# Optimization experiments

Hardware: AMD Instinct MI355X
Metric: run time of the kernel (lower is better)

The kernel has to match this reference:

```python
import jax, jax.numpy as jnp
import numpy as np

B, S, E, H = 2, 2048, 1024, 16
D = E // H  # head dimension = 64


def setup_inputs() -> dict:
    key = jax.random.key(0)
    ks = jax.random.split(key, 12)
    scale_in = 1.0 / np.sqrt(E)
    x = jax.random.normal(ks[0], (B, S, E), dtype=jnp.float32)
    # random 0/1 attention mask (1 = attend, 0 = masked out)
    mask = jax.random.randint(ks[1], (B, S, S), 0, 2, dtype=jnp.int32)
    # per-head QKV projections, stacked over the head axis: [H, E, D]
    Wq = jax.random.normal(ks[2], (H, E, D), dtype=jnp.float32) * scale_in
    bq = jnp.zeros((H, D), dtype=jnp.float32)
    Wk = jax.random.normal(ks[3], (H, E, D), dtype=jnp.float32) * scale_in
    bk = jnp.zeros((H, D), dtype=jnp.float32)
    Wv = jax.random.normal(ks[4], (H, E, D), dtype=jnp.float32) * scale_in
    bv = jnp.zeros((H, D), dtype=jnp.float32)
    # output projection: [H*D, E] == [E, E]
    Wo = jax.random.normal(ks[5], (H * D, E), dtype=jnp.float32) * scale_in
    bo = jnp.zeros((E,), dtype=jnp.float32)
    return {"x": x, "mask": mask, "Wq": Wq, "bq": bq, "Wk": Wk, "bk": bk,
            "Wv": Wv, "bv": bv, "Wo": Wo, "bo": bo}


def reference(x, mask, Wq, bq, Wk, bk, Wv, bv, Wo, bo):
    # Batched equivalent of the per-head Python loop: all heads at once.
    q = jnp.einsum('bse,hed->bhsd', x, Wq) + bq[None, :, None, :]  # [B,H,S,D]
    k = jnp.einsum('bse,hed->bhsd', x, Wk) + bk[None, :, None, :]
    v = jnp.einsum('bse,hed->bhsd', x, Wv) + bv[None, :, None, :]
    scale = 1.0 / jnp.sqrt(jnp.asarray(D, dtype=q.dtype))
    scores = jnp.einsum('bhsd,bhtd->bhst', q, k) * scale          # [B,H,S,S]
    scores = jnp.where(mask[:, None, :, :] != 0, scores, jnp.asarray(-1e9, scores.dtype))
    attn = jax.nn.softmax(scores, axis=-1)
    ctx = jnp.einsum('bhst,bhtd->bhsd', attn, v)                  # [B,H,S,D]
    # concat heads along feature dim (torch.cat(dim=2))
    concat = jnp.transpose(ctx, (0, 2, 1, 3)).reshape(B, S, H * D)
    return concat @ Wo + bo
```

## Files before the change

kernel.cpp:

```cpp
#include <hip/hip_runtime.h>

#define S_LEN 2048
#define EMB   1024
#define NH    16
#define HD    64
#define BS    2
#define QSCALE 0.18033688f

typedef __bf16 bf16;
typedef bf16  bf16x8 __attribute__((ext_vector_type(8)));
typedef bf16  bf16x4 __attribute__((ext_vector_type(4)));
typedef float f32x4  __attribute__((ext_vector_type(4)));
typedef unsigned long long u64;
typedef unsigned int u32;

__device__ __forceinline__ bf16x8 ld8(const bf16* p){ return *(const bf16x8*)p; }

__device__ __forceinline__ void gl_lds16(const bf16* g, void* l) {
    __builtin_amdgcn_global_load_lds(
        (const __attribute__((address_space(1))) void*)g,
        (__attribute__((address_space(3))) void*)l,
        16, 0, 0);
}

#define SW(row, g) ((((g) ^ ((row) & 7))) * 8)

__global__ __launch_bounds__(256)
void pack_mask(const int* __restrict__ mask, u64* __restrict__ pm)
{
    int lane = threadIdx.x & 63;
    int row  = blockIdx.x * 4 + (threadIdx.x >> 6);
    const int* mr = mask + (size_t)row * S_LEN;
    u64* pr = pm + (size_t)row * (S_LEN / 64);
    for (int i = 0; i < S_LEN / 64; ++i) {
        u64 bits = __ballot(mr[i * 64 + lane] != 0);
        if (lane == 0) pr[i] = bits;
    }
}

__global__ __launch_bounds__(256)
void transpose_w(const float* __restrict__ W0, const float* __restrict__ W1,
                 const float* __restrict__ W2, const float* __restrict__ W3,
                 bf16* __restrict__ Wt)
{
    const int z = blockIdx.z;
    const float* W = z == 0 ? W0 : z == 1 ? W1 : z == 2 ? W2 : W3;
    const bool head = z < 3;
    const int k0 = blockIdx.x * 64, n0 = blockIdx.y * 64;
    const int tid = threadIdx.x;
    __shared__ float T[64][68];
    {
        int k = k0 + (tid >> 2), cg = (tid & 3) * 16;
        size_t base = head ? ((size_t)(n0 >> 6) * ((size_t)EMB * HD) + (size_t)k * HD + cg)
                           : ((size_t)k * EMB + n0 + cg);
        #pragma unroll
        for (int g = 0; g < 4; ++g) {
            f32x4 v = *(const f32x4*)(W + base + g * 4);
            #pragma unroll
            for (int j = 0; j < 4; ++j) T[tid >> 2][cg + g * 4 + j] = v[j];
        }
    }
    __syncthreads();
    {
        int n = n0 + (tid >> 2), ck = (tid & 3) * 16;
        bf16 t16[16];
        #pragma unroll
        for (int j = 0; j < 16; ++j) t16[j] = (bf16)T[ck + j][tid >> 2];
        bf16* outp = Wt + (size_t)z * EMB * EMB + (size_t)n * EMB + k0 + ck;
        *(bf16x8*)outp       = *(bf16x8*)t16;
        *(bf16x8*)(outp + 8) = *(bf16x8*)(t16 + 8);
    }
}

__global__ __launch_bounds__(256)
void cvt_f32_bf16(const float* __restrict__ x, bf16* __restrict__ y)
{
    size_t i = ((size_t)blockIdx.x * 256 + threadIdx.x) * 16;
    bf16 t[16];
    #pragma unroll
    for (int g = 0; g < 4; ++g) {
        f32x4 v = *(const f32x4*)(x + i + g * 4);
        #pragma unroll
        for (int j = 0; j < 4; ++j) t[g * 4 + j] = (bf16)v[j];
    }
    *(bf16x8*)(y + i)     = *(bf16x8*)t;
    *(bf16x8*)(y + i + 8) = *(bf16x8*)(t + 8);
}

__global__ __launch_bounds__(256)
void scale_q(bf16* __restrict__ q)
{
    size_t i = ((size_t)blockIdx.x * 256 + threadIdx.x) * 8;
    bf16x8 v = *(bf16x8*)(q + i);
    #pragma unroll
    for (int j = 0; j < 8; ++j) v[j] = (bf16)((float)v[j] * QSCALE);
    *(bf16x8*)(q + i) = v;
}

__global__ __launch_bounds__(256, 3)
void gemm_qkv(const void* __restrict__ Ap, const bf16* __restrict__ Wt,
              const float* __restrict__ bqp, const float* __restrict__ bkp,
              const float* __restrict__ bvp,
              bf16* __restrict__ qb, bf16* __restrict__ kb, bf16* __restrict__ VT,
              int a32)
{
    const int tid  = threadIdx.x;
    const int lane = tid & 63, quad = lane >> 4, c = lane & 15;
    const int w = tid >> 6, wm = w >> 1, wn = w & 1;
    const int m0 = blockIdx.x * 128;
    const int n0 = blockIdx.y * 128;

    __shared__ bf16 Ash[128][64];
    __shared__ bf16 Wsh[128][64];

    f32x4 acc[4][4];
    #pragma unroll
    for (int mt = 0; mt < 4; ++mt)
        #pragma unroll
        for (int nt = 0; nt < 4; ++nt) acc[mt][nt] = (f32x4){0.f,0.f,0.f,0.f};

    const int lrow = lane >> 3, lcol = (lane & 7) * 8;

    for (int k0 = 0; k0 < EMB; k0 += 64) {
        __syncthreads();
        if (!a32) {
            const bf16* A = (const bf16*)Ap;
            #pragma unroll
            for (int j = 0; j < 4; ++j)
                gl_lds16(A + (size_t)(m0 + w * 32 + j * 8 + lrow) * EMB + k0 + lcol,
                         &Ash[w * 32 + j * 8][0]);
        } else {
            const float* A = (const float*)Ap + (size_t)(m0 + (tid >> 1)) * EMB + k0 + (tid & 1) * 32;
            bf16 t[32];
            #pragma unroll
            for (int g = 0; g < 8; ++g) {
                f32x4 v = *(const f32x4*)(A + g * 4);
                #pragma unroll
                for (int j = 0; j < 4; ++j) t[g * 4 + j] = (bf16)v[j];
            }
            #pragma unroll
            for (int g2 = 0; g2 < 4; ++g2)
                *(bf16x8*)&Ash[tid >> 1][(tid & 1) * 32 + g2 * 8] = *(bf16x8*)(t + g2 * 8);
        }
        #pragma unroll
        for (int j = 0; j < 4; ++j)
            gl_lds16(Wt + (size_t)(n0 + w * 32 + j * 8 + lrow) * EMB + k0 + lcol,
                     &Wsh[w * 32 + j * 8][0]);
        __syncthreads();

        #pragma unroll
        for (int kh = 0; kh < 2; ++kh) {
            bf16x8 af[4], bfv[4];
            #pragma unroll
            for (int mt = 0; mt < 4; ++mt) af[mt]  = ld8(&Ash[wm * 64 + mt * 16 + c][kh * 32 + quad * 8]);
            #pragma unroll
            for (int nt = 0; nt < 4; ++nt) bfv[nt] = ld8(&Wsh[wn * 64 + nt * 16 + c][kh * 32 + quad * 8]);
            #pragma unroll
            for (int mt = 0; mt < 4; ++mt)
                #pragma unroll
                for (int nt = 0; nt < 4; ++nt)
                    acc[mt][nt] = __builtin_amdgcn_mfma_f32_16x16x32_bf16(af[mt], bfv[nt], acc[mt][nt], 0, 0, 0);
        }
    }

    const int z = n0 >> 10;
    const float* bias = z == 0 ? bqp : z == 1 ? bkp : bvp;
    #pragma unroll
    for (int nt = 0; nt < 4; ++nt) {
        int nn = (n0 & 1023) + wn * 64 + nt * 16 + c;
        float bv_ = bias[nn];
        #pragma unroll
        for (int mt = 0; mt < 4; ++mt)
            #pragma unroll
            for (int r = 0; r < 4; ++r) {
                int m = m0 + wm * 64 + mt * 16 + quad * 4 + r;
                float v = acc[mt][nt][r] + bv_;
                if (z == 0)      qb[(size_t)m * EMB + nn] = (bf16)(v * QSCALE);
                else if (z == 1) kb[(size_t)m * EMB + nn] = (bf16)v;
                else {
                    int head = nn >> 6, d = nn & 63;
                    VT[((size_t)((m >> 11) * NH + head) * HD + d) * S_LEN + (m & 2047)] = (bf16)v;
                }
            }
    }
}

__global__ __launch_bounds__(256, 4)
void gemm_o(const bf16* __restrict__ Ap, const bf16* __restrict__ Wt,
            const float* __restrict__ bo, float* __restrict__ C)
{
    const int tid  = threadIdx.x;
    const int lane = tid & 63, quad = lane >> 4, c = lane & 15;
    const int w = tid >> 6, wm = w >> 1, wn = w & 1;
    const int m0 = blockIdx.x * 128;
    const int n0 = blockIdx.y * 64;

    __shared__ bf16 Ash[128][64];
    __shared__ bf16 Wsh[64][64];

    f32x4 acc[4][2];
    #pragma unroll
    for (int mt = 0; mt < 4; ++mt)
        #pragma unroll
        for (int nt = 0; nt < 2; ++nt) acc[mt][nt] = (f32x4){0.f,0.f,0.f,0.f};

    const int lrow = lane >> 3, lcol = (lane & 7) * 8;

    for (int k0 = 0; k0 < EMB; k0 += 64) {
        __syncthreads();
        #pragma unroll
        for (int j = 0; j < 4; ++j)
            gl_lds16(Ap + (size_t)(m0 + w * 32 + j * 8 + lrow) * EMB + k0 + lcol,
                     &Ash[w * 32 + j * 8][0]);
        #pragma unroll
        for (int j = 0; j < 2; ++j)
            gl_lds16(Wt + (size_t)(n0 + w * 16 + j * 8 + lrow) * EMB + k0 + lcol,
                     &Wsh[w * 16 + j * 8][0]);
        __syncthreads();

        #pragma unroll
        for (int kh = 0; kh < 2; ++kh) {
            bf16x8 af[4], bfv[2];
            #pragma unroll
            for (int mt = 0; mt < 4; ++mt) af[mt]  = ld8(&Ash[wm * 64 + mt * 16 + c][kh * 32 + quad * 8]);
            #pragma unroll
            for (int nt = 0; nt < 2; ++nt) bfv[nt] = ld8(&Wsh[wn * 32 + nt * 16 + c][kh * 32 + quad * 8]);
            #pragma unroll
            for (int mt = 0; mt < 4; ++mt)
                #pragma unroll
                for (int nt = 0; nt < 2; ++nt)
                    acc[mt][nt] = __builtin_amdgcn_mfma_f32_16x16x32_bf16(af[mt], bfv[nt], acc[mt][nt], 0, 0, 0);
        }
    }

    #pragma unroll
    for (int nt = 0; nt < 2; ++nt) {
        int n = n0 + wn * 32 + nt * 16 + c;
        float bv_ = bo[n];
        #pragma unroll
        for (int mt = 0; mt < 4; ++mt)
            #pragma unroll
            for (int r = 0; r < 4; ++r) {
                int m = m0 + wm * 64 + mt * 16 + quad * 4 + r;
                C[(size_t)m * EMB + n] = acc[mt][nt][r] + bv_;
            }
    }
}

__global__ __launch_bounds__(512)
void gemm128(const void* __restrict__ Ap, const float* __restrict__ Wp,
             const bf16* __restrict__ Wtp, const float* __restrict__ bias,
             void* __restrict__ Cp, int N, int K, int whead,
             int m_base, int a32, int cmode)
{
    const int tid  = threadIdx.x;
    const int lane = tid & 63, quad = lane >> 4, c = lane & 15;
    const int w = tid >> 6, wm = w >> 2, wn = w & 3;
    const int m0 = blockIdx.x * 128, n0 = blockIdx.y * 128;

    __shared__ bf16 Ash[128][64];
    __shared__ bf16 Wsh[128][64];

    f32x4 acc[4][2];
    #pragma unroll
    for (int mt = 0; mt < 4; ++mt)
        #pragma unroll
        for (int nt = 0; nt < 2; ++nt) acc[mt][nt] = (f32x4){0.f,0.f,0.f,0.f};

    const int arow = tid >> 2, aq = tid & 3;

    auto compute = [&]() {
        #pragma unroll
        for (int kh = 0; kh < 2; ++kh) {
            bf16x8 bfr[2];
            #pragma unroll
            for (int nt = 0; nt < 2; ++nt) {
                int rw = wn * 32 + nt * 16 + c;
                bfr[nt] = ld8(&Wsh[rw][SW(rw, kh * 4 + quad)]);
            }
            #pragma unroll
            for (int mt = 0; mt < 4; ++mt) {
                int ra = wm * 64 + mt * 16 + c;
                bf16x8 af = ld8(&Ash[ra][SW(ra, kh * 4 + quad)]);
                #pragma unroll
                for (int nt = 0; nt < 2; ++nt)
                    acc[mt][nt] = __builtin_amdgcn_mfma_f32_16x16x32_bf16(af, bfr[nt], acc[mt][nt], 0, 0, 0);
            }
        }
    };

    for (int k0 = 0; k0 < K; k0 += 64) {
        __syncthreads();
        if (a32) {
            const float* A = (const float*)Ap + (size_t)(m_base + m0 + arow) * K + k0 + aq * 16;
            bf16 t16[16];
            #pragma unroll
            for (int g = 0; g < 4; ++g) {
                f32x4 v = *(const f32x4*)(A + g * 4);
                #pragma unroll
                for (int j = 0; j < 4; ++j) t16[g * 4 + j] = (bf16)v[j];
            }
            *(bf16x8*)&Ash[arow][SW(arow, aq * 2)]     = *(bf16x8*)t16;
            *(bf16x8*)&Ash[arow][SW(arow, aq * 2 + 1)] = *(bf16x8*)(t16 + 8);
        } else {
            const bf16* A = (const bf16*)Ap + (size_t)(m_base + m0 + arow) * K + k0 + aq * 16;
            *(bf16x8*)&Ash[arow][SW(arow, aq * 2)]     = ld8(A);
            *(bf16x8*)&Ash[arow][SW(arow, aq * 2 + 1)] = ld8(A + 8);
        }
        {
            int nl = tid & 127, kg = tid >> 7;
            int n = n0 + nl;
            size_t base    = whead ? ((size_t)(n >> 6) * ((size_t)K * HD) + (n & 63))
                                   : (size_t)n;
            size_t kstride = whead ? (size_t)HD : (size_t)N;
            #pragma unroll
            for (int p = 0; p < 2; ++p) {
                int grp = kg + 4 * p;
                bf16 t8[8];
                #pragma unroll
                for (int j = 0; j < 8; ++j)
                    t8[j] = (bf16)Wp[base + (size_t)(k0 + grp * 8 + j) * kstride];
                *(bf16x8*)&Wsh[nl][SW(nl, grp)] = *(bf16x8*)t8;
            }
        }
        __syncthreads();
        compute();
    }

    #pragma unroll
    for (int nt = 0; nt < 2; ++nt) {
        int n = n0 + wn * 32 + nt * 16 + c;
        float bv_ = bias[n];
        #pragma unroll
        for (int mt = 0; mt < 4; ++mt)
            #pragma unroll
            for (int r = 0; r < 4; ++r) {
                int m = m0 + wm * 64 + mt * 16 + quad * 4 + r;
                float v = acc[mt][nt][r] + bv_;
                if (cmode == 0)      ((bf16*)Cp)[(size_t)m * N + n] = (bf16)v;
                else if (cmode == 1) ((float*)Cp)[(size_t)m * N + n] = v;
                else {
                    int mm = m_base + m;
                    ((bf16*)Cp)[((size_t)((mm >> 11) * NH + (n >> 6)) * HD + (n & 63)) * S_LEN + (mm & 2047)] = (bf16)v;
                }
            }
    }
}

__global__ __launch_bounds__(512, 2)
void attn_kernel(bf16* q0p, bf16* q1p, const bf16* __restrict__ kbuf,
                 const bf16* __restrict__ VTg, const u64* __restrict__ pmask)
{
    const int tid  = threadIdx.x;
    const int w    = tid >> 6;
    const int lane = tid & 63;
    const int quad = lane >> 4;
    const int c    = lane & 15;
    const int q0   = blockIdx.x * 128;
    const int bh   = blockIdx.y;
    const int b    = bh >> 4, h = bh & 15;

    bf16* qc = b ? q1p : q0p;
    const bf16* kh_ = kbuf + (size_t)b * S_LEN * EMB + h * HD;
    const bf16* vt  = VTg + (size_t)bh * HD * S_LEN;

    __shared__ bf16 Ksh [2][64][64];
    __shared__ bf16 VTsh[2][64][64];
    __shared__ bf16 Psh[8][16][64];

    bf16x8 qf[2];
    #pragma unroll
    for (int kk = 0; kk < 2; ++kk)
        qf[kk] = ld8(qc + (size_t)(q0 + w * 16 + c) * EMB + h * HD + kk * 32 + quad * 8);

    const u64* pmr = pmask + (size_t)(b * S_LEN + q0 + w * 16 + c) * (S_LEN / 64);

    f32x4 l4 = (f32x4){0.f,0.f,0.f,0.f};
    f32x4 o[4];
    #pragma unroll
    for (int dt = 0; dt < 4; ++dt) o[dt] = (f32x4){0.f,0.f,0.f,0.f};

    const int srow = tid >> 3, sg = tid & 7;
    bf16x8 kr, vr;
    auto loadKV = [&](int t0) {
        kr = ld8(kh_ + (size_t)(t0 + srow) * EMB + sg * 8);
        vr = ld8(vt + (size_t)srow * S_LEN + t0 + sg * 8);
    };

    loadKV(0);
    int buf = 0;
    for (int t0 = 0; t0 < S_LEN; t0 += 64) {
        *(bf16x8*)&Ksh [buf][srow][SW(srow, sg)] = kr;
        *(bf16x8*)&VTsh[buf][srow][SW(srow, sg)] = vr;
        __syncthreads();
        if (t0 + 64 < S_LEN) loadKV(t0 + 64);

        u64 s0 = pmr[t0 >> 6] >> (quad * 4);
        u32 mm[2] = {(u32)s0, (u32)(s0 >> 32)};

        f32x4 sc[4];
        #pragma unroll
        for (int tt = 0; tt < 4; ++tt) sc[tt] = (f32x4){0.f,0.f,0.f,0.f};
        #pragma unroll
        for (int tt = 0; tt < 4; ++tt)
            #pragma unroll
            for (int kk = 0; kk < 2; ++kk) {
                int rk = tt * 16 + c;
                bf16x8 ka = ld8(&Ksh[buf][rk][SW(rk, kk * 4 + quad)]);
                sc[tt] = __builtin_amdgcn_mfma_f32_16x16x32_bf16(ka, qf[kk], sc[tt], 0, 0, 0);
            }

        #pragma unroll
        for (int tt = 0; tt < 4; ++tt) {
            u32 half = mm[tt >> 1];
            bf16x4 pv;
            #pragma unroll
            for (int r = 0; r < 4; ++r) {
                float e = __builtin_amdgcn_exp2f(sc[tt][r]);
                e = ((half >> ((tt & 1) * 16 + r)) & 1) ? e : 0.f;
                l4[r] += e;
                pv[r] = (bf16)e;
            }
            *(bf16x4*)&Psh[w][c][SW(c, tt * 2 + (quad >> 1)) + (quad & 1) * 4] = pv;
        }
        __builtin_amdgcn_s_waitcnt(0xc07f);

        #pragma unroll
        for (int th = 0; th < 2; ++th) {
            bf16x8 pf = ld8(&Psh[w][c][SW(c, th * 4 + quad)]);
            #pragma unroll
            for (int dt = 0; dt < 4; ++dt) {
                int rv = dt * 16 + c;
                bf16x8 av = ld8(&VTsh[buf][rv][SW(rv, th * 4 + quad)]);
                o[dt] = __builtin_amdgcn_mfma_f32_16x16x32_bf16(av, pf, o[dt], 0, 0, 0);
            }
        }
        buf ^= 1;
    }

    float ls = l4[0] + l4[1] + l4[2] + l4[3];
    ls += __shfl_xor(ls, 16);
    ls += __shfl_xor(ls, 32);
    float inv = 1.0f / fmaxf(ls, 1e-30f);
    #pragma unroll
    for (int dt = 0; dt < 4; ++dt) {
        bf16x4 ov;
        #pragma unroll
        for (int r = 0; r < 4; ++r) ov[r] = (bf16)(o[dt][r] * inv);
        *(bf16x4*)&qc[(size_t)(q0 + w * 16 + c) * EMB + h * HD + dt * 16 + quad * 4] = ov;
    }
}

extern "C" void kernel_launch(void* const* d_in, const int* in_sizes, int n_in,
                              void* d_out, int out_size, void* d_ws, size_t ws_size,
                              hipStream_t stream)
{
    const float* x    = (const float*)d_in[0];
    const int*   mask = (const int*)d_in[1];
    const float* Wq   = (const float*)d_in[2];
    const float* bq   = (const float*)d_in[3];
    const float* Wk   = (const float*)d_in[4];
    const float* bk   = (const float*)d_in[5];
    const float* Wv   = (const float*)d_in[6];
    const float* bv   = (const float*)d_in[7];
    const float* Wo   = (const float*)d_in[8];
    const float* bo   = (const float*)d_in[9];
    float* out = (float*)d_out;

    const size_t SLAB = (size_t)S_LEN * EMB;
    const size_t QB = (size_t)BS * SLAB * sizeof(bf16);
    const size_t WT = (size_t)4 * EMB * EMB * sizeof(bf16);
    const size_t PM = (size_t)BS * S_LEN * (S_LEN / 64) * 8;
    const size_t XB = (size_t)BS * SLAB * sizeof(bf16);

    bf16* VT = (bf16*)d_out;
    bf16* kb = (bf16*)d_out + BS * SLAB;

    dim3 b256(256), b512(512);
    dim3 gAtt (S_LEN / 128, BS * NH);
    dim3 gT   (EMB / 64, EMB / 64, 4);
    dim3 gPk  (BS * S_LEN / 4);
    dim3 gFull(BS * S_LEN / 128, EMB / 128);
    dim3 gHalf(S_LEN / 128, EMB / 128);

    if (ws_size >= QB + WT + PM + 64) {
        bf16* qb  = (bf16*)d_ws;
        bf16* Wt  = (bf16*)((char*)d_ws + QB);
        u64*  pm  = (u64*)((char*)d_ws + QB + WT);
        const void* xA = x; int a32 = 1;
        if (ws_size >= QB + WT + PM + XB + 64) {
            bf16* xbf = (bf16*)((char*)d_ws + QB + WT + PM);
            cvt_f32_bf16<<<dim3(1024), b256, 0, stream>>>(x, xbf);
            xA = xbf; a32 = 0;
        }
        pack_mask<<<gPk, b256, 0, stream>>>(mask, pm);
        transpose_w<<<gT, b256, 0, stream>>>(Wq, Wk, Wv, Wo, Wt);

        gemm_qkv<<<dim3(BS * S_LEN / 128, 3 * EMB / 128), b256, 0, stream>>>(
            xA, Wt, bq, bk, bv, qb, kb, VT, a32);

        attn_kernel<<<gAtt, b512, 0, stream>>>(qb, qb + SLAB, kb, VT, pm);

        gemm_o<<<dim3(BS * S_LEN / 128, EMB / 64), b256, 0, stream>>>(
            qb, Wt + (size_t)3 * EMB * EMB, bo, out);
    } else if (ws_size >= QB + PM + 64) {
        bf16* qb = (bf16*)d_ws;
        u64*  pm = (u64*)((char*)d_ws + QB);
        pack_mask<<<gPk, b256, 0, stream>>>(mask, pm);

        gemm128<<<gFull, b512, 0, stream>>>(x, Wk, nullptr, bk, kb, EMB, EMB, 1, 0, 1, 0);
        gemm128<<<gFull, b512, 0, stream>>>(x, Wv, nullptr, bv, VT, EMB, EMB, 1, 0, 1, 2);
        gemm128<<<gFull, b512, 0, stream>>>(x, Wq, nullptr, bq, qb, EMB, EMB, 1, 0, 1, 0);
        scale_q<<<dim3(BS * SLAB / (256 * 8)), b256, 0, stream>>>(qb);

        attn_kernel<<<gAtt, b512, 0, stream>>>(qb, qb + SLAB, kb, VT, pm);

        gemm128<<<gFull, b512, 0, stream>>>(qb, Wo, nullptr, bo, out, EMB, EMB, 0, 0, 0, 1);
    } else {
        bf16* qb0 = (bf16*)d_in[4];
        bf16* qb1 = (bf16*)d_in[6];
        u64*  pm  = (u64*)d_in[2];

        gemm128<<<gFull, b512, 0, stream>>>(x, Wk, nullptr, bk, kb, EMB, EMB, 1, 0, 1, 0);
        gemm128<<<gFull, b512, 0, stream>>>(x, Wv, nullptr, bv, VT, EMB, EMB, 1, 0, 1, 2);
        gemm128<<<gHalf, b512, 0, stream>>>(x, Wq, nullptr, bq, qb0, EMB, EMB, 1, 0,     1, 0);
        gemm128<<<gHalf, b512, 0, stream>>>(x, Wq, nullptr, bq, qb1, EMB, EMB, 1, S_LEN, 1, 0);
        scale_q<<<dim3(SLAB / (256 * 8)), b256, 0, stream>>>(qb0);
        scale_q<<<dim3(SLAB / (256 * 8)), b256, 0, stream>>>(qb1);
        pack_mask<<<gPk, b256, 0, stream>>>(mask, pm);

        attn_kernel<<<gAtt, b512, 0, stream>>>(qb0, qb1, kb, VT, pm);

        gemm128<<<gHalf, b512, 0, stream>>>(qb0, Wo, nullptr, bo, out,        EMB, EMB, 0, 0, 0, 1);
        gemm128<<<gHalf, b512, 0, stream>>>(qb1, Wo, nullptr, bo, out + SLAB, EMB, EMB, 0, 0, 0, 1);
    }
}
```

Before: 242.2 us.

## Restructure attention: 4 waves with 32 rows each, P kept in registers

The attention kernel now uses 256 threads, with each wave handling two 16-row query tiles, so every K/V fragment read from LDS feeds two MFMAs. The P matrix no longer goes through shared memory. It stays in registers in the 16x16x16 MFMA operand layout, with V^T read as 4-element fragments matching that layout. s_setprio hints are placed around the MFMA sections. In exchange, per-thread register use is higher and each block does more KV loading per thread, which changes occupancy (launch bounds 256,3).

Result: slower. 257.5 us (+6.3%).

```diff
diff --git a/kernel.cpp b/kernel.cpp
--- a/kernel.cpp
+++ b/kernel.cpp
@@ -11,6 +11,7 @@
 typedef bf16  bf16x8 __attribute__((ext_vector_type(8)));
 typedef bf16  bf16x4 __attribute__((ext_vector_type(4)));
 typedef float f32x4  __attribute__((ext_vector_type(4)));
+typedef short s16x4  __attribute__((ext_vector_type(4)));
 typedef unsigned long long u64;
 typedef unsigned int u32;
 
@@ -347,7 +348,7 @@
     }
 }
 
-__global__ __launch_bounds__(512, 2)
+__global__ __launch_bounds__(256, 3)
 void attn_kernel(bf16* q0p, bf16* q1p, const bf16* __restrict__ kbuf,
                  const bf16* __restrict__ VTg, const u64* __restrict__ pmask)
 {
@@ -366,88 +367,115 @@
 
     __shared__ bf16 Ksh [2][64][64];
     __shared__ bf16 VTsh[2][64][64];
-    __shared__ bf16 Psh[8][16][64];
-
-    bf16x8 qf[2];
-    #pragma unroll
-    for (int kk = 0; kk < 2; ++kk)
-        qf[kk] = ld8(qc + (size_t)(q0 + w * 16 + c) * EMB + h * HD + kk * 32 + quad * 8);
-
-    const u64* pmr = pmask + (size_t)(b * S_LEN + q0 + w * 16 + c) * (S_LEN / 64);
-
-    f32x4 l4 = (f32x4){0.f,0.f,0.f,0.f};
-    f32x4 o[4];
-    #pragma unroll
-    for (int dt = 0; dt < 4; ++dt) o[dt] = (f32x4){0.f,0.f,0.f,0.f};
-
-    const int srow = tid >> 3, sg = tid & 7;
-    bf16x8 kr, vr;
+
+    bf16x8 qf[2][2];
+    #pragma unroll
+    for (int rq = 0; rq < 2; ++rq)
+        #pragma unroll
+        for (int kk = 0; kk < 2; ++kk)
+            qf[rq][kk] = ld8(qc + (size_t)(q0 + w * 32 + rq * 16 + c) * EMB + h * HD + kk * 32 + quad * 8);
+
+    const u64* pmr0 = pmask + (size_t)(b * S_LEN + q0 + w * 32 + c) * (S_LEN / 64);
+    const u64* pmr1 = pmr0 + (size_t)16 * (S_LEN / 64);
+
+    f32x4 l4[2];
+    f32x4 o[2][4];
+    #pragma unroll
+    for (int rq = 0; rq < 2; ++rq) {
+        l4[rq] = (f32x4){0.f,0.f,0.f,0.f};
+        #pragma unroll
+        for (int dt = 0; dt < 4; ++dt) o[rq][dt] = (f32x4){0.f,0.f,0.f,0.f};
+    }
+
+    const int srow = tid >> 2, sg2 = (tid & 3) * 2;
+    bf16x8 kr0, kr1, vr0, vr1;
     auto loadKV = [&](int t0) {
-        kr = ld8(kh_ + (size_t)(t0 + srow) * EMB + sg * 8);
-        vr = ld8(vt + (size_t)srow * S_LEN + t0 + sg * 8);
+        const bf16* kp = kh_ + (size_t)(t0 + srow) * EMB + sg2 * 8;
+        kr0 = ld8(kp); kr1 = ld8(kp + 8);
+        const bf16* vp = vt + (size_t)srow * S_LEN + t0 + sg2 * 8;
+        vr0 = ld8(vp); vr1 = ld8(vp + 8);
     };
 
     loadKV(0);
     int buf = 0;
     for (int t0 = 0; t0 < S_LEN; t0 += 64) {
-        *(bf16x8*)&Ksh [buf][srow][SW(srow, sg)] = kr;
-        *(bf16x8*)&VTsh[buf][srow][SW(srow, sg)] = vr;
+        *(bf16x8*)&Ksh [buf][srow][SW(srow, sg2)]     = kr0;
+        *(bf16x8*)&Ksh [buf][srow][SW(srow, sg2 + 1)] = kr1;
+        *(bf16x8*)&VTsh[buf][srow][SW(srow, sg2)]     = vr0;
+        *(bf16x8*)&VTsh[buf][srow][SW(srow, sg2 + 1)] = vr1;
         __syncthreads();
         if (t0 + 64 < S_LEN) loadKV(t0 + 64);
 
-        u64 s0 = pmr[t0 >> 6] >> (quad * 4);
-        u32 mm[2] = {(u32)s0, (u32)(s0 >> 32)};
-
-        f32x4 sc[4];
-        #pragma unroll
-        for (int tt = 0; tt < 4; ++tt) sc[tt] = (f32x4){0.f,0.f,0.f,0.f};
+        u64 s0[2] = { pmr0[t0 >> 6] >> (quad * 4), pmr1[t0 >> 6] >> (quad * 4) };
+
+        f32x4 sc[4][2];
         #pragma unroll
         for (int tt = 0; tt < 4; ++tt)
             #pragma unroll
-            for (int kk = 0; kk < 2; ++kk) {
+            for (int rq = 0; rq < 2; ++rq) sc[tt][rq] = (f32x4){0.f,0.f,0.f,0.f};
+        __builtin_amdgcn_s_setprio(1);
+        #pragma unroll
+        for (int kk = 0; kk < 2; ++kk)
+            #pragma unroll
+            for (int tt = 0; tt < 4; ++tt) {
                 int rk = tt * 16 + c;
                 bf16x8 ka = ld8(&Ksh[buf][rk][SW(rk, kk * 4 + quad)]);
-                sc[tt] = __builtin_amdgcn_mfma_f32_16x16x32_bf16(ka, qf[kk], sc[tt], 0, 0, 0);
-            }
-
-        #pragma unroll
-        for (int tt = 0; tt < 4; ++tt) {
-            u32 half = mm[tt >> 1];
-            bf16x4 pv;
-            #pragma unroll
-            for (int r = 0; r < 4; ++r) {
-                float e = __builtin_amdgcn_exp2f(sc[tt][r]);
-                e = ((half >> ((tt & 1) * 16 + r)) & 1) ? e : 0.f;
-                l4[r] += e;
-                pv[r] = (bf16)e;
-            }
-            *(bf16x4*)&Psh[w][c][SW(c, tt * 2 + (quad >> 1)) + (quad & 1) * 4] = pv;
-        }
-        __builtin_amdgcn_s_waitcnt(0xc07f);
-
-        #pragma unroll
-        for (int th = 0; th < 2; ++th) {
-            bf16x8 pf = ld8(&Psh[w][c][SW(c, th * 4 + quad)]);
-            #pragma unroll
-            for (int dt = 0; dt < 4; ++dt) {
-                int rv = dt * 16 + c;
-                bf16x8 av = ld8(&VTsh[buf][rv][SW(rv, th * 4 + quad)]);
-                o[dt] = __builtin_amdgcn_mfma_f32_16x16x32_bf16(av, pf, o[dt], 0, 0, 0);
-            }
-        }
+                #pragma unroll
+                for (int rq = 0; rq < 2; ++rq)
+                    sc[tt][rq] = __builtin_amdgcn_mfma_f32_16x16x32_bf16(ka, qf[rq][kk], sc[tt][rq], 0, 0, 0);
+            }
+        __builtin_amdgcn_s_setprio(0);
+
+        s16x4 p[4][2];
+        #pragma unroll
+        for (int rq = 0; rq < 2; ++rq) {
+            u32 mm0 = (u32)s0[rq], mm1 = (u32)(s0[rq] >> 32);
+            #pragma unroll
+            for (int tt = 0; tt < 4; ++tt) {
+                u32 half = (tt & 2) ? mm1 : mm0;
+                bf16x4 pv;
+                #pragma unroll
+                for (int r = 0; r < 4; ++r) {
+                    float e = __builtin_amdgcn_exp2f(sc[tt][rq][r]);
+                    e = ((half >> ((tt & 1) * 16 + r)) & 1) ? e : 0.f;
+                    l4[rq][r] += e;
+                    pv[r] = (bf16)e;
+                }
+                p[tt][rq] = __builtin_bit_cast(s16x4, pv);
+            }
+        }
+
+        __builtin_amdgcn_s_setprio(1);
+        #pragma unroll
+        for (int dt = 0; dt < 4; ++dt) {
+            int rv = dt * 16 + c;
+            #pragma unroll
+            for (int tt = 0; tt < 4; ++tt) {
+                int g = tt * 2 + (quad >> 1);
+                s16x4 av = __builtin_bit_cast(s16x4,
+                    *(const bf16x4*)&VTsh[buf][rv][((g ^ (rv & 7)) * 8) + (quad & 1) * 4]);
+                #pragma unroll
+                for (int rq = 0; rq < 2; ++rq)
+                    o[rq][dt] = __builtin_amdgcn_mfma_f32_16x16x16bf16_1k(av, p[tt][rq], o[rq][dt], 0, 0, 0);
+            }
+        }
+        __builtin_amdgcn_s_setprio(0);
         buf ^= 1;
     }
 
-    float ls = l4[0] + l4[1] + l4[2] + l4[3];
-    ls += __shfl_xor(ls, 16);
-    ls += __shfl_xor(ls, 32);
-    float inv = 1.0f / fmaxf(ls, 1e-30f);
-    #pragma unroll
-    for (int dt = 0; dt < 4; ++dt) {
-        bf16x4 ov;
-        #pragma unroll
-        for (int r = 0; r < 4; ++r) ov[r] = (bf16)(o[dt][r] * inv);
-        *(bf16x4*)&qc[(size_t)(q0 + w * 16 + c) * EMB + h * HD + dt * 16 + quad * 4] = ov;
+    #pragma unroll
+    for (int rq = 0; rq < 2; ++rq) {
+        float ls = l4[rq][0] + l4[rq][1] + l4[rq][2] + l4[rq][3];
+        ls += __shfl_xor(ls, 16);
+        ls += __shfl_xor(ls, 32);
+        float inv = 1.0f / fmaxf(ls, 1e-30f);
+        #pragma unroll
+        for (int dt = 0; dt < 4; ++dt) {
+            bf16x4 ov;
+            #pragma unroll
+            for (int r = 0; r < 4; ++r) ov[r] = (bf16)(o[rq][dt][r] * inv);
+            *(bf16x4*)&qc[(size_t)(q0 + w * 32 + rq * 16 + c) * EMB + h * HD + dt * 16 + quad * 4] = ov;
+        }
     }
 }
 
@@ -499,7 +527,7 @@
         gemm_qkv<<<dim3(BS * S_LEN / 128, 3 * EMB / 128), b256, 0, stream>>>(
             xA, Wt, bq, bk, bv, qb, kb, VT, a32);
 
-        attn_kernel<<<gAtt, b512, 0, stream>>>(qb, qb + SLAB, kb, VT, pm);
+        attn_kernel<<<gAtt, b256, 0, stream>>>(qb, qb + SLAB, kb, VT, pm);
 
         gemm_o<<<dim3(BS * S_LEN / 128, EMB / 64), b256, 0, stream>>>(
             qb, Wt + (size_t)3 * EMB * EMB, bo, out);
@@ -513,7 +541,7 @@
         gemm128<<<gFull, b512, 0, stream>>>(x, Wq, nullptr, bq, qb, EMB, EMB, 1, 0, 1, 0);
         scale_q<<<dim3(BS * SLAB / (256 * 8)), b256, 0, stream>>>(qb);
 
-        attn_kernel<<<gAtt, b512, 0, stream>>>(qb, qb + SLAB, kb, VT, pm);
+        attn_kernel<<<gAtt, b256, 0, stream>>>(qb, qb + SLAB, kb, VT, pm);
 
         gemm128<<<gFull, b512, 0, stream>>>(qb, Wo, nullptr, bo, out, EMB, EMB, 0, 0, 0, 1);
     } else {
@@ -529,7 +557,7 @@
         scale_q<<<dim3(SLAB / (256 * 8)), b256, 0, stream>>>(qb1);
         pack_mask<<<gPk, b256, 0, stream>>>(mask, pm);
 
-        attn_kernel<<<gAtt, b512, 0, stream>>>(qb0, qb1, kb, VT, pm);
+        attn_kernel<<<gAtt, b256, 0, stream>>>(qb0, qb1, kb, VT, pm);
 
         gemm128<<<gHalf, b512, 0, stream>>>(qb0, Wo, nullptr, bo, out,        EMB, EMB, 0, 0, 0, 1);
         gemm128<<<gHalf, b512, 0, stream>>>(qb1, Wo, nullptr, bo, out + SLAB, EMB, EMB, 0, 0, 0, 1);
```
